# Kernel optimization log

Measured on AMD Instinct MI355X. Metric: run time of the kernel, lower is better.

## Reference

```python
import jax, jax.numpy as jnp
import numpy as np

DIM = 96
EXPANSION = 2
INNER = DIM * EXPANSION        # 192
QKV_BLOCK = 4                  # per-head dim DH
NH = INNER // QKV_BLOCK        # 48 heads
CONV_K = 4
B, H, W = 2, 24, 24
EPS = 1e-5


def setup_inputs() -> dict:
    key = jax.random.key(0)
    ks = jax.random.split(key, 10)
    nrm = lambda k, shape, s=0.02: jax.random.normal(k, shape, dtype=jnp.float32) * s
    return {
        "x": jax.random.normal(ks[0], (B, DIM, H, W), dtype=jnp.float32),
        "ln_g": jnp.ones((DIM,), jnp.float32),
        "ln_b": jnp.zeros((DIM,), jnp.float32),
        "w_up": nrm(ks[1], (2 * INNER, DIM)),
        "b_up": jnp.zeros((2 * INNER,), jnp.float32),
        "w_q": nrm(ks[2], (NH, QKV_BLOCK, QKV_BLOCK), 0.2),
        "b_q": jnp.zeros((INNER,), jnp.float32),
        "w_k": nrm(ks[3], (NH, QKV_BLOCK, QKV_BLOCK), 0.2),
        "b_k": jnp.zeros((INNER,), jnp.float32),
        "w_v": nrm(ks[4], (NH, QKV_BLOCK, QKV_BLOCK), 0.2),
        "b_v": jnp.zeros((INNER,), jnp.float32),
        "w_conv": nrm(ks[5], (INNER, 1, CONV_K), 0.1),  # depthwise (O,I/g,K)
        "b_conv": jnp.zeros((INNER,), jnp.float32),
        "w_ig": nrm(ks[6], (NH, 3 * INNER)),
        "b_ig": jnp.zeros((NH,), jnp.float32),
        "w_fg": jnp.zeros((NH, 3 * INNER), jnp.float32),
        "b_fg": jnp.linspace(3.0, 6.0, NH, dtype=jnp.float32),  # xLSTM fgate bias init
        "on_g": jnp.ones((INNER,), jnp.float32),
        "on_b": jnp.zeros((INNER,), jnp.float32),
        "skip": jnp.ones((INNER,), jnp.float32),
        "w_down": nrm(ks[7], (DIM, INNER)),
        "b_down": jnp.zeros((DIM,), jnp.float32),
    }


def _layernorm(x, g, b):
    m = x.mean(-1, keepdims=True)
    v = x.var(-1, keepdims=True)
    return (x - m) / jnp.sqrt(v + EPS) * g + b


def _causal_conv(x, w, b):
    # x: (B,S,D); depthwise causal conv1d, left-pad K-1
    y = jax.lax.conv_general_dilated(
        x.transpose(0, 2, 1), w, (1,), [(CONV_K - 1, 0)],
        feature_group_count=INNER, dimension_numbers=("NCH", "OIH", "NCH"))
    return y.transpose(0, 2, 1) + b


def _headwise(x, w, b):
    # LinearHeadwiseExpand: block-diagonal per-head linear
    Bq, S, _ = x.shape
    xh = x.reshape(Bq, S, NH, QKV_BLOCK)
    return jnp.einsum("bsnd,nod->bsno", xh, w).reshape(Bq, S, INNER) + b


def _mlstm(q, k, v, ig, fg):
    # parallel_stabilized_simple; q,k,v: (B,NH,S,DH); ig,fg: (B,NH,S)
    S, DH = q.shape[2], q.shape[3]
    log_f = jax.nn.log_sigmoid(fg)                                           # (B,NH,S)
    lf_cum = jnp.concatenate(
        [jnp.zeros_like(log_f[..., :1]), jnp.cumsum(log_f, axis=-1)], axis=-1)  # (B,NH,S+1)
    log_fmat = lf_cum[..., :, None] - lf_cum[..., None, :]                   # (B,NH,S+1,S+1)
    ltr = jnp.tril(jnp.ones((S, S), dtype=bool))
    log_fg_mat = jnp.where(ltr, log_fmat[..., 1:, 1:], -jnp.inf)             # (B,NH,S,S)
    log_D = log_fg_mat + ig[..., None, :]
    max_log_D = jnp.max(log_D, axis=-1, keepdims=True)                       # rowwise stabilizer
    Dm = jnp.exp(log_D - max_log_D)
    qk = jnp.einsum("bhsd,bhtd->bhst", q, k) * (DH ** -0.5)
    Cm = qk * Dm
    normalizer = jnp.maximum(jnp.abs(Cm.sum(-1, keepdims=True)), jnp.exp(-max_log_D))
    return jnp.einsum("bhst,bhtd->bhsd", Cm / (normalizer + 1e-6), v)


def _mh_norm(h, g, b):
    # MultiHeadLayerNorm: per-head normalization over DH, then full affine
    m = h.mean(-1, keepdims=True)
    v = h.var(-1, keepdims=True)
    hn = (h - m) / jnp.sqrt(v + EPS)
    return hn * g.reshape(1, NH, 1, QKV_BLOCK) + b.reshape(1, NH, 1, QKV_BLOCK)


def reference(x, ln_g, ln_b, w_up, b_up, w_q, b_q, w_k, b_k, w_v, b_v,
              w_conv, b_conv, w_ig, b_ig, w_fg, b_fg, on_g, on_b, skip,
              w_down, b_down):
    Bb, C, Hh, Ww = x.shape
    S = Hh * Ww
    xs = x.reshape(Bb, C, S).transpose(0, 2, 1)                 # (B,S,C)
    h = _layernorm(xs, ln_g, ln_b)                              # ViLBlock pre-LN
    xi = h @ w_up.T + b_up                                      # (B,S,2*INNER)
    x_mlstm, z = jnp.split(xi, 2, axis=-1)
    x_conv = jax.nn.silu(_causal_conv(x_mlstm, w_conv, b_conv))
    q = _headwise(x_conv, w_q, b_q)
    k = _headwise(x_conv, w_k, b_k)
    v = _headwise(x_mlstm, w_v, b_v)
    qkv = jnp.concatenate([q, k, v], axis=-1)                   # (B,S,3*INNER)
    ig = jnp.einsum("bsf,hf->bhs", qkv, w_ig) + b_ig[None, :, None]
    fg = jnp.einsum("bsf,hf->bhs", qkv, w_fg) + b_fg[None, :, None]
    to_heads = lambda t: t.reshape(Bb, S, NH, QKV_BLOCK).transpose(0, 2, 1, 3)
    h_tilde = _mlstm(to_heads(q), to_heads(k), to_heads(v), ig, fg)   # (B,NH,S,DH)
    h_norm = _mh_norm(h_tilde, on_g, on_b).transpose(0, 2, 1, 3).reshape(Bb, S, INNER)
    h_skip = h_norm + skip * x_conv
    h_state = h_skip * jax.nn.silu(z)
    out = h_state @ w_down.T + b_down
    y = xs + out                                                # ViLBlock residual
    return y.transpose(0, 2, 1).reshape(Bb, C, Hh, Ww)
```

## Files before the change

kernel.cpp:

```cpp
#include <hip/hip_runtime.h>
#include <math.h>

#define SEQ   576
#define CDIM  96
#define INNER 192
#define NHEAD 48
#define DH    4
#define NB    2
#define EPSV  1e-5f
#define RT    64

__device__ __forceinline__ float silu_f(float x) { return x / (1.f + __expf(-x)); }
__device__ __forceinline__ float logsig_f(float x) {
    return (x >= 0.f) ? -log1pf(__expf(-x)) : (x - log1pf(__expf(x)));
}

__global__ void __launch_bounds__(512) k_ln_up(const float* __restrict__ x,
    const float* __restrict__ ln_g, const float* __restrict__ ln_b,
    const float* __restrict__ w_up, const float* __restrict__ b_up,
    float* __restrict__ xm, float* __restrict__ z) {
    const int t = threadIdx.x;
    const int p0 = blockIdx.x * 8;
    const int b = p0 / SEQ;
    const int f0 = blockIdx.y * 192;
    __shared__ __align__(16) float hbuf[8][CDIM];

    {
        const int p = t >> 6, l = t & 63;
        const int s = (p0 + p) % SEQ;
        const float v0 = x[(size_t)(b * CDIM + l) * SEQ + s];
        const float v1 = (l < 32) ? x[(size_t)(b * CDIM + 64 + l) * SEQ + s] : 0.f;
        float sum = v0 + v1, sq = v0 * v0 + v1 * v1;
        #pragma unroll
        for (int off = 1; off < 64; off <<= 1) {
            sum += __shfl_xor(sum, off);
            sq  += __shfl_xor(sq, off);
        }
        const float mean = sum * (1.f / CDIM);
        const float var = sq * (1.f / CDIM) - mean * mean;
        const float rstd = rsqrtf(var + EPSV);
        hbuf[p][l] = (v0 - mean) * rstd * ln_g[l] + ln_b[l];
        if (l < 32) hbuf[p][64 + l] = (v1 - mean) * rstd * ln_g[64 + l] + ln_b[64 + l];
    }
    __syncthreads();

    const int lane = t & 7, oi = t >> 3;
    const int p2 = oi & 7, fg = oi >> 3;
    const int pos = p0 + p2;
    const float4* hr = (const float4*)(&hbuf[p2][0]) + lane * 3;
    const float4 h0 = hr[0], h1 = hr[1], h2 = hr[2];
    #pragma unroll 4
    for (int j = 0; j < 24; ++j) {
        const int f = f0 + fg + 8 * j;
        const float4* wr = (const float4*)(w_up + (size_t)f * CDIM) + lane * 3;
        float4 w0 = wr[0], w1 = wr[1], w2 = wr[2];
        float acc = h0.x * w0.x + h0.y * w0.y + h0.z * w0.z + h0.w * w0.w
                  + h1.x * w1.x + h1.y * w1.y + h1.z * w1.z + h1.w * w1.w
                  + h2.x * w2.x + h2.y * w2.y + h2.z * w2.z + h2.w * w2.w;
        #pragma unroll
        for (int off = 1; off < 8; off <<= 1) acc += __shfl_xor(acc, off);
        if (lane == 0) {
            acc += b_up[f];
            if (f < INNER) xm[(size_t)pos * INNER + f] = acc;
            else           z [(size_t)pos * INNER + (f - INNER)] = acc;
        }
    }
}

__global__ void __launch_bounds__(512) k_conv_qkv_gates(const float* __restrict__ xm,
    const float* __restrict__ w_conv, const float* __restrict__ b_conv,
    const float* __restrict__ w_q, const float* __restrict__ b_q,
    const float* __restrict__ w_k, const float* __restrict__ b_k,
    const float* __restrict__ w_v, const float* __restrict__ b_v,
    const float* __restrict__ w_ig, const float* __restrict__ b_ig,
    const float* __restrict__ w_fg, const float* __restrict__ b_fg,
    float* __restrict__ xc, float* __restrict__ qw, float* __restrict__ kw,
    float* __restrict__ vw, float* __restrict__ igw, float* __restrict__ fgw) {
    const int t = threadIdx.x;
    const int p0 = blockIdx.x * 4;
    const int b = p0 / SEQ, s0 = p0 % SEQ;
    __shared__ float xmb[7][INNER];
    __shared__ float xcb[4][INNER];
    __shared__ __align__(16) float qkvb[4][3 * INNER];

    for (int i = t; i < 7 * INNER; i += 512) {
        const int r = i / INNER, c = i % INNER;
        const int ss = s0 - 3 + r;
        xmb[r][c] = (ss >= 0) ? xm[(size_t)(b * SEQ + ss) * INNER + c] : 0.f;
    }
    __syncthreads();

    for (int i = t; i < 4 * INNER; i += 512) {
        const int p = i / INNER, c = i % INNER;
        float acc = b_conv[c];
        #pragma unroll
        for (int j = 0; j < 4; ++j) acc += xmb[p + j][c] * w_conv[c * 4 + j];
        const float v = silu_f(acc);
        xcb[p][c] = v;
        xc[(size_t)(b * SEQ + s0 + p) * INNER + c] = v;
    }
    __syncthreads();

    for (int i = t; i < 4 * INNER; i += 512) {
        const int p = i / INNER, c = i % INNER;
        const int n = c >> 2, o = c & 3;
        const float* wq = w_q + n * 16 + o * 4;
        const float* wk = w_k + n * 16 + o * 4;
        const float* wv = w_v + n * 16 + o * 4;
        float q = b_q[c], k = b_k[c], v = b_v[c];
        #pragma unroll
        for (int dd = 0; dd < 4; ++dd) {
            q += xcb[p][n * 4 + dd] * wq[dd];
            k += xcb[p][n * 4 + dd] * wk[dd];
            v += xmb[p + 3][n * 4 + dd] * wv[dd];
        }
        qkvb[p][c] = q; qkvb[p][INNER + c] = k; qkvb[p][2 * INNER + c] = v;
        const size_t base = ((size_t)(b * NHEAD + n) * SEQ + s0 + p) * DH + o;
        qw[base] = q; kw[base] = k; vw[base] = v;
    }
    __syncthreads();

    {
        const int w = t >> 6;
        const int l16 = t & 15, gg = (t >> 4) & 3;
        #pragma unroll
        for (int it = 0; it < 3; ++it) {
            const int g = w * 12 + it * 4 + gg;
            const bool isfg = (g >= NHEAD);
            const int hh = isfg ? (g - NHEAD) : g;
            const float4* wr = (const float4*)((isfg ? w_fg : w_ig) + (size_t)hh * (3 * INNER)) + l16 * 9;
            float4 wf[9];
            #pragma unroll
            for (int j = 0; j < 9; ++j) wf[j] = wr[j];
            #pragma unroll
            for (int p = 0; p < 4; ++p) {
                const float4* xr = (const float4*)(&qkvb[p][0]) + l16 * 9;
                float acc = 0.f;
                #pragma unroll
                for (int j = 0; j < 9; ++j) {
                    const float4 a = xr[j];
                    acc += a.x * wf[j].x + a.y * wf[j].y + a.z * wf[j].z + a.w * wf[j].w;
                }
                #pragma unroll
                for (int off = 1; off < 16; off <<= 1) acc += __shfl_xor(acc, off);
                if (l16 == 0) {
                    acc += isfg ? b_fg[hh] : b_ig[hh];
                    (isfg ? fgw : igw)[((size_t)b * NHEAD + hh) * SEQ + s0 + p] = acc;
                }
            }
        }
    }
}

__global__ void __launch_bounds__(256) k_mlstm(const float* __restrict__ qw,
    const float* __restrict__ kw, const float* __restrict__ vw,
    const float* __restrict__ igw, const float* __restrict__ fgw,
    float* __restrict__ ht) {
    const int bh = blockIdx.x;
    const int r0 = blockIdx.y * RT;
    const int nt = r0 + RT;
    const int t = threadIdx.x;
    __shared__ float4 k4[SEQ], v4[SEQ];
    __shared__ float m_l[SEQ], M_l[SEQ], lfc_l[SEQ];

    const float4* kb = (const float4*)(kw + (size_t)bh * SEQ * DH);
    const float4* vb = (const float4*)(vw + (size_t)bh * SEQ * DH);
    for (int i = t; i < nt; i += 256) { k4[i] = kb[i]; v4[i] = vb[i]; }

    if (t < 64) {
        const int base = t * 9;
        float pre[9], mv[9], mx[9];
        float run = 0.f;
        #pragma unroll
        for (int j = 0; j < 9; ++j) {
            run += logsig_f(fgw[(size_t)bh * SEQ + base + j]);
            pre[j] = run;
        }
        float incl = run;
        #pragma unroll
        for (int off = 1; off < 64; off <<= 1) {
            float o = __shfl_up(incl, off);
            if (t >= off) incl += o;
        }
        const float excl = incl - run;
        float runm = -INFINITY;
        #pragma unroll
        for (int j = 0; j < 9; ++j) {
            float lfc = excl + pre[j];
            lfc_l[base + j] = lfc;
            float mt = igw[(size_t)bh * SEQ + base + j] - lfc;
            mv[j] = mt;
            runm = fmaxf(runm, mt);
            mx[j] = runm;
        }
        float sc = runm;
        #pragma unroll
        for (int off = 1; off < 64; off <<= 1) {
            float o = __shfl_up(sc, off);
            if (t >= off) sc = fmaxf(sc, o);
        }
        float exclm = __shfl_up(sc, 1);
        if (t == 0) exclm = -INFINITY;
        #pragma unroll
        for (int j = 0; j < 9; ++j) {
            m_l[base + j] = mv[j];
            M_l[base + j] = fmaxf(exclm, mx[j]);
        }
    }
    __syncthreads();

    const int sub = t & 3;
    const int s0 = r0 + (t >> 2);
    const float4 q = ((const float4*)(qw + (size_t)bh * SEQ * DH))[s0];
    const float Ms = M_l[s0], lfcs = lfc_l[s0];

    float a0 = 0.f, a1 = 0.f, a2 = 0.f, a3 = 0.f, csum = 0.f;
    for (int tt = sub; tt <= s0; tt += 4) {
        float e = __expf(m_l[tt] - Ms);
        float4 kk = k4[tt], vv = v4[tt];
        float qk = q.x * kk.x + q.y * kk.y + q.z * kk.z + q.w * kk.w;
        float c = qk * 0.5f * e;
        csum += c;
        a0 += c * vv.x; a1 += c * vv.y; a2 += c * vv.z; a3 += c * vv.w;
    }
    #pragma unroll
    for (int off = 1; off < 4; off <<= 1) {
        csum += __shfl_xor(csum, off);
        a0 += __shfl_xor(a0, off); a1 += __shfl_xor(a1, off);
        a2 += __shfl_xor(a2, off); a3 += __shfl_xor(a3, off);
    }
    const float floorv = __expf(-(lfcs + Ms));
    const float inv = 1.f / (fmaxf(fabsf(csum), floorv) + 1e-6f);
    const float val = (sub == 0) ? a0 : (sub == 1) ? a1 : (sub == 2) ? a2 : a3;
    ht[((size_t)bh * SEQ + s0) * 4 + sub] = val * inv;
}

__global__ void __launch_bounds__(512) k_epi(const float* __restrict__ ht,
    const float* __restrict__ on_g, const float* __restrict__ on_b,
    const float* __restrict__ skip, const float* __restrict__ xc,
    const float* __restrict__ zz, const float* __restrict__ w_down,
    const float* __restrict__ b_down, const float* __restrict__ x,
    float* __restrict__ out) {
    const int t = threadIdx.x;
    const int p0 = blockIdx.x * 4;
    const int b = p0 / SEQ;
    __shared__ __align__(16) float hs[4][INNER];

    for (int i = t; i < 4 * INNER; i += 512) {
        const int p = i / INNER, c = i % INNER;
        const int pos = p0 + p, s = pos % SEQ;
        const int n = c >> 2, o = c & 3;
        const float4 hv = ((const float4*)ht)[(size_t)(b * NHEAD + n) * SEQ + s];
        const float mean = (hv.x + hv.y + hv.z + hv.w) * 0.25f;
        const float d0 = hv.x - mean, d1 = hv.y - mean, d2 = hv.z - mean, d3 = hv.w - mean;
        const float var = (d0 * d0 + d1 * d1 + d2 * d2 + d3 * d3) * 0.25f;
        const float rstd = rsqrtf(var + EPSV);
        const float he = (o == 0) ? hv.x : (o == 1) ? hv.y : (o == 2) ? hv.z : hv.w;
        const float hn = (he - mean) * rstd * on_g[c] + on_b[c];
        const float hk = hn + skip[c] * xc[(size_t)pos * INNER + c];
        hs[p][c] = hk * silu_f(zz[(size_t)pos * INNER + c]);
    }
    __syncthreads();

    const int lane = t & 7, oi = t >> 3;
    const int p2 = oi & 3, cg = oi >> 2;
    const int pos = p0 + p2, s = pos % SEQ;
    const float4* hr = (const float4*)(&hs[p2][0]) + lane * 6;
    float4 h4[6];
    #pragma unroll
    for (int j = 0; j < 6; ++j) h4[j] = hr[j];
    #pragma unroll
    for (int j = 0; j < 6; ++j) {
        const int c = cg + 16 * j;
        const float4* wr = (const float4*)(w_down + (size_t)c * INNER) + lane * 6;
        float acc = 0.f;
        #pragma unroll
        for (int u = 0; u < 6; ++u) {
            const float4 w = wr[u];
            acc += h4[u].x * w.x + h4[u].y * w.y + h4[u].z * w.z + h4[u].w * w.w;
        }
        #pragma unroll
        for (int off = 1; off < 8; off <<= 1) acc += __shfl_xor(acc, off);
        if (lane == 0) {
            const size_t idx = ((size_t)b * CDIM + c) * SEQ + s;
            out[idx] = x[idx] + acc + b_down[c];
        }
    }
}

extern "C" void kernel_launch(void* const* d_in, const int* in_sizes, int n_in,
                              void* d_out, int out_size, void* d_ws, size_t ws_size,
                              hipStream_t stream) {
    const float* x      = (const float*)d_in[0];
    const float* ln_g   = (const float*)d_in[1];
    const float* ln_b   = (const float*)d_in[2];
    const float* w_up   = (const float*)d_in[3];
    const float* b_up   = (const float*)d_in[4];
    const float* w_q    = (const float*)d_in[5];
    const float* b_q    = (const float*)d_in[6];
    const float* w_k    = (const float*)d_in[7];
    const float* b_k    = (const float*)d_in[8];
    const float* w_v    = (const float*)d_in[9];
    const float* b_v    = (const float*)d_in[10];
    const float* w_conv = (const float*)d_in[11];
    const float* b_conv = (const float*)d_in[12];
    const float* w_ig   = (const float*)d_in[13];
    const float* b_ig   = (const float*)d_in[14];
    const float* w_fg   = (const float*)d_in[15];
    const float* b_fg   = (const float*)d_in[16];
    const float* on_g   = (const float*)d_in[17];
    const float* on_b   = (const float*)d_in[18];
    const float* skip   = (const float*)d_in[19];
    const float* w_down = (const float*)d_in[20];
    const float* b_down = (const float*)d_in[21];

    float* ws = (float*)d_ws;
    const size_t NSI = (size_t)NB * SEQ * INNER;
    const size_t NHS = (size_t)NB * NHEAD * SEQ;
    float* xm  = ws;
    float* z   = xm + NSI;
    float* xc  = z + NSI;
    float* qw  = xc + NSI;
    float* kw  = qw + NSI;
    float* vw  = kw + NSI;
    float* igw = vw + NSI;
    float* fgw = igw + NHS;
    float* ht  = fgw + NHS;

    float* out = (float*)d_out;

    hipLaunchKernelGGL(k_ln_up, dim3(NB * SEQ / 8, 2), dim3(512), 0, stream,
                       x, ln_g, ln_b, w_up, b_up, xm, z);
    hipLaunchKernelGGL(k_conv_qkv_gates, dim3(NB * SEQ / 4), dim3(512), 0, stream,
                       xm, w_conv, b_conv, w_q, b_q, w_k, b_k, w_v, b_v,
                       w_ig, b_ig, w_fg, b_fg, xc, qw, kw, vw, igw, fgw);
    hipLaunchKernelGGL(k_mlstm, dim3(NB * NHEAD, SEQ / RT), dim3(256), 0, stream,
                       qw, kw, vw, igw, fgw, ht);
    hipLaunchKernelGGL(k_epi, dim3(NB * SEQ / 4), dim3(512), 0, stream,
                       ht, on_g, on_b, skip, xc, z, w_down, b_down, x, out);
}
```

Before: 60.31 us.

## Widen parallel split across LN-up, mLSTM and epilogue kernels

The up-projection grid now splits the output features four ways instead of two, so each block computes 12 features per thread group instead of 24. The mLSTM kernel moves to 512 threads, with 8 lanes per query row instead of 4, and lane 0 writes a single float4 result per row. The epilogue handles 2 positions per 256-thread block instead of 4 per 512. The aim is more blocks and shorter per-thread loops to hide latency on a small problem. The cost is more redundant LayerNorm and weight loads, and a longer shuffle reduction in mLSTM.

```diff
diff --git a/kernel.cpp b/kernel.cpp
--- a/kernel.cpp
+++ b/kernel.cpp
@@ -22,8 +22,8 @@
     const int t = threadIdx.x;
     const int p0 = blockIdx.x * 8;
     const int b = p0 / SEQ;
-    const int f0 = blockIdx.y * 192;
-    __shared__ __align__(16) float hbuf[8][CDIM];
+    const int f0 = blockIdx.y * 96;
+    __shared__ __align__(16) float hbuf[8 * CDIM];
 
     {
         const int p = t >> 6, l = t & 63;
@@ -37,26 +37,25 @@
             sq  += __shfl_xor(sq, off);
         }
         const float mean = sum * (1.f / CDIM);
-        const float var = sq * (1.f / CDIM) - mean * mean;
-        const float rstd = rsqrtf(var + EPSV);
-        hbuf[p][l] = (v0 - mean) * rstd * ln_g[l] + ln_b[l];
-        if (l < 32) hbuf[p][64 + l] = (v1 - mean) * rstd * ln_g[64 + l] + ln_b[64 + l];
+        const float rstd = rsqrtf(sq * (1.f / CDIM) - mean * mean + EPSV);
+        hbuf[p * CDIM + l] = (v0 - mean) * rstd * ln_g[l] + ln_b[l];
+        if (l < 32) hbuf[p * CDIM + 64 + l] = (v1 - mean) * rstd * ln_g[64 + l] + ln_b[64 + l];
     }
     __syncthreads();
 
     const int lane = t & 7, oi = t >> 3;
     const int p2 = oi & 7, fg = oi >> 3;
     const int pos = p0 + p2;
-    const float4* hr = (const float4*)(&hbuf[p2][0]) + lane * 3;
+    const float4* hr = (const float4*)(hbuf + p2 * CDIM) + lane * 3;
     const float4 h0 = hr[0], h1 = hr[1], h2 = hr[2];
     #pragma unroll 4
-    for (int j = 0; j < 24; ++j) {
+    for (int j = 0; j < 12; ++j) {
         const int f = f0 + fg + 8 * j;
         const float4* wr = (const float4*)(w_up + (size_t)f * CDIM) + lane * 3;
-        float4 w0 = wr[0], w1 = wr[1], w2 = wr[2];
-        float acc = h0.x * w0.x + h0.y * w0.y + h0.z * w0.z + h0.w * w0.w
-                  + h1.x * w1.x + h1.y * w1.y + h1.z * w1.z + h1.w * w1.w
-                  + h2.x * w2.x + h2.y * w2.y + h2.z * w2.z + h2.w * w2.w;
+        const float4 w0 = wr[0], w1 = wr[1], w2 = wr[2];
+        float acc = h0.x*w0.x + h0.y*w0.y + h0.z*w0.z + h0.w*w0.w
+                  + h1.x*w1.x + h1.y*w1.y + h1.z*w1.z + h1.w*w1.w
+                  + h2.x*w2.x + h2.y*w2.y + h2.z*w2.z + h2.w*w2.w;
         #pragma unroll
         for (int off = 1; off < 8; off <<= 1) acc += __shfl_xor(acc, off);
         if (lane == 0) {
@@ -121,14 +120,13 @@
     __syncthreads();
 
     {
-        const int w = t >> 6;
-        const int l16 = t & 15, gg = (t >> 4) & 3;
+        const int w = t >> 6, l16 = t & 15, gg = (t >> 4) & 3;
         #pragma unroll
         for (int it = 0; it < 3; ++it) {
             const int g = w * 12 + it * 4 + gg;
             const bool isfg = (g >= NHEAD);
             const int hh = isfg ? (g - NHEAD) : g;
-            const float4* wr = (const float4*)((isfg ? w_fg : w_ig) + (size_t)hh * (3 * INNER)) + l16 * 9;
+            const float4* wr = (const float4*)((isfg ? w_fg : w_ig) + (size_t)hh * 576) + l16 * 9;
             float4 wf[9];
             #pragma unroll
             for (int j = 0; j < 9; ++j) wf[j] = wr[j];
@@ -152,7 +150,7 @@
     }
 }
 
-__global__ void __launch_bounds__(256) k_mlstm(const float* __restrict__ qw,
+__global__ void __launch_bounds__(512) k_mlstm(const float* __restrict__ qw,
     const float* __restrict__ kw, const float* __restrict__ vw,
     const float* __restrict__ igw, const float* __restrict__ fgw,
     float* __restrict__ ht) {
@@ -165,7 +163,7 @@
 
     const float4* kb = (const float4*)(kw + (size_t)bh * SEQ * DH);
     const float4* vb = (const float4*)(vw + (size_t)bh * SEQ * DH);
-    for (int i = t; i < nt; i += 256) { k4[i] = kb[i]; v4[i] = vb[i]; }
+    for (int i = t; i < nt; i += 512) { k4[i] = kb[i]; v4[i] = vb[i]; }
 
     if (t < 64) {
         const int base = t * 9;
@@ -209,51 +207,52 @@
     }
     __syncthreads();
 
-    const int sub = t & 3;
-    const int s0 = r0 + (t >> 2);
+    const int lane = t & 7;
+    const int s0 = r0 + (t >> 3);
     const float4 q = ((const float4*)(qw + (size_t)bh * SEQ * DH))[s0];
     const float Ms = M_l[s0], lfcs = lfc_l[s0];
 
     float a0 = 0.f, a1 = 0.f, a2 = 0.f, a3 = 0.f, csum = 0.f;
-    for (int tt = sub; tt <= s0; tt += 4) {
-        float e = __expf(m_l[tt] - Ms);
-        float4 kk = k4[tt], vv = v4[tt];
-        float qk = q.x * kk.x + q.y * kk.y + q.z * kk.z + q.w * kk.w;
-        float c = qk * 0.5f * e;
+    for (int tt = lane; tt <= s0; tt += 8) {
+        const float e = __expf(m_l[tt] - Ms);
+        const float4 kk = k4[tt], vv = v4[tt];
+        const float c = (q.x*kk.x + q.y*kk.y + q.z*kk.z + q.w*kk.w) * 0.5f * e;
         csum += c;
         a0 += c * vv.x; a1 += c * vv.y; a2 += c * vv.z; a3 += c * vv.w;
     }
     #pragma unroll
-    for (int off = 1; off < 4; off <<= 1) {
+    for (int off = 1; off < 8; off <<= 1) {
         csum += __shfl_xor(csum, off);
         a0 += __shfl_xor(a0, off); a1 += __shfl_xor(a1, off);
         a2 += __shfl_xor(a2, off); a3 += __shfl_xor(a3, off);
     }
-    const float floorv = __expf(-(lfcs + Ms));
-    const float inv = 1.f / (fmaxf(fabsf(csum), floorv) + 1e-6f);
-    const float val = (sub == 0) ? a0 : (sub == 1) ? a1 : (sub == 2) ? a2 : a3;
-    ht[((size_t)bh * SEQ + s0) * 4 + sub] = val * inv;
-}
-
-__global__ void __launch_bounds__(512) k_epi(const float* __restrict__ ht,
+    if (lane == 0) {
+        const float floorv = __expf(-(lfcs + Ms));
+        const float inv = 1.f / (fmaxf(fabsf(csum), floorv) + 1e-6f);
+        ((float4*)ht)[(size_t)bh * SEQ + s0] =
+            make_float4(a0 * inv, a1 * inv, a2 * inv, a3 * inv);
+    }
+}
+
+__global__ void __launch_bounds__(256) k_epi(const float* __restrict__ ht,
     const float* __restrict__ on_g, const float* __restrict__ on_b,
     const float* __restrict__ skip, const float* __restrict__ xc,
     const float* __restrict__ zz, const float* __restrict__ w_down,
     const float* __restrict__ b_down, const float* __restrict__ x,
     float* __restrict__ out) {
     const int t = threadIdx.x;
-    const int p0 = blockIdx.x * 4;
+    const int p0 = blockIdx.x * 2;
     const int b = p0 / SEQ;
-    __shared__ __align__(16) float hs[4][INNER];
-
-    for (int i = t; i < 4 * INNER; i += 512) {
+    __shared__ __align__(16) float hs[2][INNER];
+
+    for (int i = t; i < 2 * INNER; i += 256) {
         const int p = i / INNER, c = i % INNER;
         const int pos = p0 + p, s = pos % SEQ;
         const int n = c >> 2, o = c & 3;
         const float4 hv = ((const float4*)ht)[(size_t)(b * NHEAD + n) * SEQ + s];
         const float mean = (hv.x + hv.y + hv.z + hv.w) * 0.25f;
         const float d0 = hv.x - mean, d1 = hv.y - mean, d2 = hv.z - mean, d3 = hv.w - mean;
-        const float var = (d0 * d0 + d1 * d1 + d2 * d2 + d3 * d3) * 0.25f;
+        const float var = (d0*d0 + d1*d1 + d2*d2 + d3*d3) * 0.25f;
         const float rstd = rsqrtf(var + EPSV);
         const float he = (o == 0) ? hv.x : (o == 1) ? hv.y : (o == 2) ? hv.z : hv.w;
         const float hn = (he - mean) * rstd * on_g[c] + on_b[c];
@@ -263,7 +262,7 @@
     __syncthreads();
 
     const int lane = t & 7, oi = t >> 3;
-    const int p2 = oi & 3, cg = oi >> 2;
+    const int p2 = oi & 1, cg2 = oi >> 1;
     const int pos = p0 + p2, s = pos % SEQ;
     const float4* hr = (const float4*)(&hs[p2][0]) + lane * 6;
     float4 h4[6];
@@ -271,13 +270,13 @@
     for (int j = 0; j < 6; ++j) h4[j] = hr[j];
     #pragma unroll
     for (int j = 0; j < 6; ++j) {
-        const int c = cg + 16 * j;
+        const int c = cg2 + 16 * j;
         const float4* wr = (const float4*)(w_down + (size_t)c * INNER) + lane * 6;
         float acc = 0.f;
         #pragma unroll
         for (int u = 0; u < 6; ++u) {
             const float4 w = wr[u];
-            acc += h4[u].x * w.x + h4[u].y * w.y + h4[u].z * w.z + h4[u].w * w.w;
+            acc += h4[u].x*w.x + h4[u].y*w.y + h4[u].z*w.z + h4[u].w*w.w;
         }
         #pragma unroll
         for (int off = 1; off < 8; off <<= 1) acc += __shfl_xor(acc, off);
@@ -329,13 +328,13 @@
 
     float* out = (float*)d_out;
 
-    hipLaunchKernelGGL(k_ln_up, dim3(NB * SEQ / 8, 2), dim3(512), 0, stream,
+    hipLaunchKernelGGL(k_ln_up, dim3(NB * SEQ / 8, 4), dim3(512), 0, stream,
                        x, ln_g, ln_b, w_up, b_up, xm, z);
     hipLaunchKernelGGL(k_conv_qkv_gates, dim3(NB * SEQ / 4), dim3(512), 0, stream,
                        xm, w_conv, b_conv, w_q, b_q, w_k, b_k, w_v, b_v,
                        w_ig, b_ig, w_fg, b_fg, xc, qw, kw, vw, igw, fgw);
-    hipLaunchKernelGGL(k_mlstm, dim3(NB * NHEAD, SEQ / RT), dim3(256), 0, stream,
+    hipLaunchKernelGGL(k_mlstm, dim3(NB * NHEAD, SEQ / RT), dim3(512), 0, stream,
                        qw, kw, vw, igw, fgw, ht);
-    hipLaunchKernelGGL(k_epi, dim3(NB * SEQ / 4), dim3(512), 0, stream,
+    hipLaunchKernelGGL(k_epi, dim3(NB * SEQ / 2), dim3(256), 0, stream,
                        ht, on_g, on_b, skip, xc, z, w_down, b_down, x, out);
 }
```

Result: faster. 55.31 us (-8.3%).
